# Kernel optimization log

Measured on AMD Instinct MI355X. Metric: run time of the kernel, lower is better.

Reference implementation:

```python
import jax, jax.numpy as jnp
import numpy as np

NUM_USERS = 100000
NUM_BOOKS = 50000
N_NODES = NUM_USERS + NUM_BOOKS
LATENT = 64
NUM_LAYERS = 3
N_EDGES = 2400000


def setup_inputs() -> dict:
    key = jax.random.key(0)
    ks = jax.random.split(key, 12)
    edge_index = jax.random.randint(ks[0], (2, N_EDGES), 0, N_NODES)
    embedding = jax.random.normal(ks[1], (N_NODES, LATENT), dtype=jnp.float32) * 0.1
    user_features = jax.random.normal(ks[2], (NUM_USERS, 16), dtype=jnp.float32)
    book_numerical_features = jax.random.normal(ks[3], (NUM_BOOKS, 8), dtype=jnp.float32)
    book_genre_features = jax.random.normal(ks[4], (NUM_BOOKS, 32), dtype=jnp.float32)
    W_user = jax.random.normal(ks[5], (16, LATENT), dtype=jnp.float32) * 0.1
    b_user = jnp.zeros((LATENT,), dtype=jnp.float32)
    W_num = jax.random.normal(ks[6], (8, LATENT), dtype=jnp.float32) * 0.1
    b_num = jnp.zeros((LATENT,), dtype=jnp.float32)
    W_genre = jax.random.normal(ks[7], (32, LATENT), dtype=jnp.float32) * 0.1
    b_genre = jnp.zeros((LATENT,), dtype=jnp.float32)
    return {
        "edge_index": edge_index,
        "embedding": embedding,
        "user_features": user_features,
        "book_numerical_features": book_numerical_features,
        "book_genre_features": book_genre_features,
        "W_user": W_user, "b_user": b_user,
        "W_num": W_num, "b_num": b_num,
        "W_genre": W_genre, "b_genre": b_genre,
    }


def reference(edge_index, embedding, user_features, book_numerical_features,
              book_genre_features, W_user, b_user, W_num, b_num, W_genre, b_genre):
    N = embedding.shape[0]
    # feature projections fused into initial embedding (emb0)
    user_proj = user_features @ W_user + b_user                       # [Nu, D]
    book_proj = (book_numerical_features @ W_num + b_num
                 + book_genre_features @ W_genre + b_genre)           # [Nb, D]
    emb0 = embedding + jnp.concatenate([user_proj, book_proj], axis=0)  # [N, D]

    frm, to = edge_index[0], edge_index[1]
    # symmetric degree normalization: deg counts incoming edges at target nodes
    deg = jax.ops.segment_sum(jnp.ones_like(to, dtype=emb0.dtype), to, num_segments=N)
    deg_inv_sqrt = jnp.where(deg > 0, deg ** -0.5, 0.0)
    norm = deg_inv_sqrt[frm] * deg_inv_sqrt[to]                       # [E]

    # LightGCN: gather -> scale -> scatter-add, then mean over all layer outputs
    emb = emb0
    acc = emb0
    for _ in range(NUM_LAYERS):
        msg = norm[:, None] * emb[frm]                                # [E, D]
        emb = jax.ops.segment_sum(msg, to, num_segments=N)            # [N, D]
        acc = acc + emb
    out = acc / (NUM_LAYERS + 1)
    return emb0, out
```

## Files before the change

### kernel.cpp

```cpp
#include <hip/hip_runtime.h>
#include <hip/hip_bf16.h>

typedef __hip_bfloat16 bf16;

#define D 64
#define BSH 8
#define CAP 5120
#define EPB 4096
#define NPW 8


__global__ __launch_bounds__(256) void k_initcur(int* __restrict__ gcur, int nbk) {
    int i = blockIdx.x * 256 + threadIdx.x;
    if (i < nbk) gcur[i] = i * CAP;
}


__global__ __launch_bounds__(256) void k_part(const int* __restrict__ frm,
                                              const int* __restrict__ to,
                                              int* __restrict__ gcur,
                                              int* __restrict__ be, int E, int nbk) {
    __shared__ int h[1024];
    int tid = threadIdx.x;
    for (int i = tid; i < 1024; i += 256) h[i] = 0;
    __syncthreads();

    int base = blockIdx.x * EPB;
    int  f[16], bk[16], tl[16];
    bool va[16];
    #pragma unroll
    for (int k = 0; k < 16; k++) {
        int i = base + k * 256 + tid;
        va[k] = (i < E);
        int ic = va[k] ? i : 0;
        int t = to[ic];
        f[k]  = frm[ic];
        bk[k] = t >> BSH;
        tl[k] = t & 255;
        if (va[k]) atomicAdd(&h[bk[k]], 1);
    }
    __syncthreads();
    for (int b = tid; b < nbk; b += 256) {
        int c = h[b];
        h[b] = (c > 0) ? atomicAdd(&gcur[b], c) : 0;
    }
    __syncthreads();
    #pragma unroll
    for (int k = 0; k < 16; k++) {
        if (va[k]) {
            int pos = atomicAdd(&h[bk[k]], 1);
            be[pos] = (f[k] << 8) | tl[k];
        }
    }
}


__global__ void k_bscan(const int* __restrict__ gcur, int* __restrict__ bstart,
                        int* __restrict__ row_start, int nbk, int N, int E) {
    __shared__ int s[1024];
    int t = threadIdx.x;
    int x = (t < nbk) ? (gcur[t] - t * CAP) : 0;
    s[t] = x;
    __syncthreads();
    #pragma unroll
    for (int off = 1; off < 1024; off <<= 1) {
        int v = s[t] + ((t >= off) ? s[t - off] : 0);
        __syncthreads();
        s[t] = v;
        __syncthreads();
    }
    if (t < nbk) bstart[t] = s[t] - x;
    if (t == 0) row_start[N] = E;
}


__global__ __launch_bounds__(256) void k_scatter(const int* __restrict__ gcur,
                                                 const int* __restrict__ bstart,
                                                 const int* __restrict__ be,
                                                 int* __restrict__ row_start,
                                                 float* __restrict__ dis,
                                                 int* __restrict__ csr, int N) {
    __shared__ int hist[256];
    __shared__ int scn[256];
    int b = blockIdx.x;
    int t = threadIdx.x;
    hist[t] = 0;
    __syncthreads();

    int base = b * CAP;
    int cnt  = gcur[b] - base;
    for (int i = t; i < cnt; i += 256)
        atomicAdd(&hist[be[base + i] & 255], 1);
    __syncthreads();

    int d = hist[t];
    scn[t] = d;
    __syncthreads();
    #pragma unroll
    for (int off = 1; off < 256; off <<= 1) {
        int v = scn[t] + ((t >= off) ? scn[t - off] : 0);
        __syncthreads();
        scn[t] = v;
        __syncthreads();
    }
    int rs = bstart[b] + (scn[t] - d);

    int node = (b << BSH) + t;
    if (node < N) {
        row_start[node] = rs;
        dis[node] = (d > 0) ? rsqrtf((float)d) : 0.0f;
    }
    hist[t] = rs;
    __syncthreads();

    for (int i = t; i < cnt; i += 256) {
        int rec = be[base + i];
        int pos = atomicAdd(&hist[rec & 255], 1);
        csr[pos] = rec >> 8;
    }
}


__global__ __launch_bounds__(256) void k_emb0(const float* __restrict__ emb,
                       const float* __restrict__ uf,
                       const float* __restrict__ bn,
                       const float* __restrict__ bg,
                       const float* __restrict__ Wu,
                       const float* __restrict__ bu,
                       const float* __restrict__ Wn,
                       const float* __restrict__ bnb,
                       const float* __restrict__ Wg,
                       const float* __restrict__ bgb,
                       const float* __restrict__ dis,
                       float* __restrict__ out0, bf16* __restrict__ y0,
                       int N, int NU, int ublocks) {
    int lane = threadIdx.x & 63;
    int wsub = __builtin_amdgcn_readfirstlane(threadIdx.x >> 6);

    if (blockIdx.x < ublocks) {
        float w[16];
        #pragma unroll
        for (int k = 0; k < 16; k++) w[k] = Wu[k * D + lane];
        float bias = bu[lane];

        int node0 = (blockIdx.x * 4 + wsub) * NPW;
        for (int n = 0; n < NPW; n++) {
            int node = node0 + n;
            if (node >= NU) break;
            const float4* f = (const float4*)(uf + (size_t)node * 16);
            float4 f0 = f[0], f1 = f[1], f2 = f[2], f3 = f[3];
            float p = bias
                + f0.x * w[0]  + f0.y * w[1]  + f0.z * w[2]  + f0.w * w[3]
                + f1.x * w[4]  + f1.y * w[5]  + f1.z * w[6]  + f1.w * w[7]
                + f2.x * w[8]  + f2.y * w[9]  + f2.z * w[10] + f2.w * w[11]
                + f3.x * w[12] + f3.y * w[13] + f3.z * w[14] + f3.w * w[15];
            size_t idx = (size_t)node * D + lane;
            float v = emb[idx] + p;
            out0[idx] = v;
            y0[idx]   = __float2bfloat16(dis[node] * v);
        }
    } else {
        float wn[8], wg[32];
        #pragma unroll
        for (int k = 0; k < 8; k++)  wn[k] = Wn[k * D + lane];
        #pragma unroll
        for (int k = 0; k < 32; k++) wg[k] = Wg[k * D + lane];
        float bias = bnb[lane] + bgb[lane];

        int b0 = ((blockIdx.x - ublocks) * 4 + wsub) * NPW;
        for (int n = 0; n < NPW; n++) {
            int b = b0 + n;
            int node = NU + b;
            if (node >= N) break;
            const float4* fn = (const float4*)(bn + (size_t)b * 8);
            float4 n0 = fn[0], n1 = fn[1];
            const float4* fg = (const float4*)(bg + (size_t)b * 32);
            float p = bias
                + n0.x * wn[0] + n0.y * wn[1] + n0.z * wn[2] + n0.w * wn[3]
                + n1.x * wn[4] + n1.y * wn[5] + n1.z * wn[6] + n1.w * wn[7];
            #pragma unroll
            for (int q = 0; q < 8; q++) {
                float4 g = fg[q];
                p += g.x * wg[4*q]   + g.y * wg[4*q+1]
                   + g.z * wg[4*q+2] + g.w * wg[4*q+3];
            }
            size_t idx = (size_t)node * D + lane;
            float v = emb[idx] + p;
            out0[idx] = v;
            y0[idx]   = __float2bfloat16(dis[node] * v);
        }
    }
}


static __device__ __forceinline__ unsigned int pack_bf16x2(float e, float o) {
    bf16 a = __float2bfloat16(e);
    bf16 b = __float2bfloat16(o);
    unsigned short ua = __builtin_bit_cast(unsigned short, a);
    unsigned short ub = __builtin_bit_cast(unsigned short, b);
    return (unsigned int)ua | ((unsigned int)ub << 16);
}


__global__ __launch_bounds__(256) void k_prop(const int* __restrict__ row_start,
                       const int* __restrict__ csr,
                       const float* __restrict__ dis,
                       const bf16* __restrict__ y_in,
                       bf16* __restrict__ x_out,
                       bf16* __restrict__ y_out, int N) {
    int lane = threadIdx.x & 63;
    int half = lane >> 5;
    int lh   = lane & 31;
    int node = blockIdx.x * 4 + (threadIdx.x >> 6);
    if (node >= N) return;

    int s = row_start[node];
    int e = row_start[node + 1];

    const unsigned int* y32 = (const unsigned int*)y_in;
    float a0 = 0.f, a1 = 0.f;

    int i = s;
    for (; i + 16 <= e; i += 16) {
        int jv = csr[i + (lane & 15)];
        #pragma unroll
        for (int u = 0; u < 8; u++) {
            int j = __shfl(jv, 2 * u + half);
            unsigned int d = y32[((unsigned int)j << 5) + lh];
            a0 += __uint_as_float(d << 16);
            a1 += __uint_as_float(d & 0xffff0000u);
        }
    }
    if (i < e) {
        int jv = csr[min(i + (lane & 15), e - 1)];
        int rem = e - i;
        for (int u = 0; 2 * u < rem; u++) {
            int idx = 2 * u + half;
            int j = __shfl(jv, idx);
            unsigned int d = y32[((unsigned int)j << 5) + lh];
            d = (idx < rem) ? d : 0u;
            a0 += __uint_as_float(d << 16);
            a1 += __uint_as_float(d & 0xffff0000u);
        }
    }

    a0 += __shfl_xor(a0, 32);
    a1 += __shfl_xor(a1, 32);

    float dt = dis[node];
    float x0 = dt * a0;
    float x1v = dt * a1;
    unsigned int w = (unsigned int)node * 32 + lh;
    if (half == 0) {
        ((unsigned int*)x_out)[w] = pack_bf16x2(x0, x1v);
    } else {
        ((unsigned int*)y_out)[w] = pack_bf16x2(dt * x0, dt * x1v);
    }
}


__global__ __launch_bounds__(256) void k_prop_last(const int* __restrict__ row_start,
                       const int* __restrict__ csr,
                       const float* __restrict__ dis,
                       const bf16* __restrict__ y_in,
                       const float* __restrict__ out0,
                       const bf16* __restrict__ x1,
                       const bf16* __restrict__ x2,
                       float* __restrict__ out1, int N) {
    int lane = threadIdx.x & 63;
    int half = lane >> 5;
    int lh   = lane & 31;
    int node = blockIdx.x * 4 + (threadIdx.x >> 6);
    if (node >= N) return;

    int s = row_start[node];
    int e = row_start[node + 1];

    const unsigned int* y32 = (const unsigned int*)y_in;
    float a0 = 0.f, a1 = 0.f;

    int i = s;
    for (; i + 16 <= e; i += 16) {
        int jv = csr[i + (lane & 15)];
        #pragma unroll
        for (int u = 0; u < 8; u++) {
            int j = __shfl(jv, 2 * u + half);
            unsigned int d = y32[((unsigned int)j << 5) + lh];
            a0 += __uint_as_float(d << 16);
            a1 += __uint_as_float(d & 0xffff0000u);
        }
    }
    if (i < e) {
        int jv = csr[min(i + (lane & 15), e - 1)];
        int rem = e - i;
        for (int u = 0; 2 * u < rem; u++) {
            int idx = 2 * u + half;
            int j = __shfl(jv, idx);
            unsigned int d = y32[((unsigned int)j << 5) + lh];
            d = (idx < rem) ? d : 0u;
            a0 += __uint_as_float(d << 16);
            a1 += __uint_as_float(d & 0xffff0000u);
        }
    }

    a0 += __shfl_xor(a0, 32);
    a1 += __shfl_xor(a1, 32);

    float dt = dis[node];
    float x3e = dt * a0;
    float x3o = dt * a1;

    if (half == 0) {
        unsigned int w = (unsigned int)node * 32 + lh;
        float2 o0 = ((const float2*)out0)[w];
        unsigned int p1 = ((const unsigned int*)x1)[w];
        unsigned int p2 = ((const unsigned int*)x2)[w];
        float e1 = __uint_as_float(p1 << 16);
        float o1 = __uint_as_float(p1 & 0xffff0000u);
        float e2 = __uint_as_float(p2 << 16);
        float o2 = __uint_as_float(p2 & 0xffff0000u);
        float2 r;
        r.x = (o0.x + e1 + e2 + x3e) * 0.25f;
        r.y = (o0.y + o1 + o2 + x3o) * 0.25f;
        ((float2*)out1)[w] = r;
    }
}


extern "C" void kernel_launch(void* const* d_in, const int* in_sizes, int n_in,
                              void* d_out, int out_size, void* d_ws, size_t ws_size,
                              hipStream_t stream) {
    const int E  = in_sizes[0] / 2;
    const int N  = in_sizes[1] / D;
    const int NU = in_sizes[2] / 16;
    const int nbk = (N + 255) >> BSH;

    const int*   frm = (const int*)d_in[0];
    const int*   to  = frm + E;
    const float* emb = (const float*)d_in[1];
    const float* uf  = (const float*)d_in[2];
    const float* bn  = (const float*)d_in[3];
    const float* bg  = (const float*)d_in[4];
    const float* Wu  = (const float*)d_in[5];
    const float* bu  = (const float*)d_in[6];
    const float* Wn  = (const float*)d_in[7];
    const float* bnb = (const float*)d_in[8];
    const float* Wg  = (const float*)d_in[9];
    const float* bgb = (const float*)d_in[10];

    char* p = (char*)d_ws;
    const size_t ND = (size_t)N * D;
    bf16*  y0        = (bf16*)p;   p += ND * sizeof(bf16);
    bf16*  y1        = (bf16*)p;   p += ND * sizeof(bf16);
    bf16*  x1        = (bf16*)p;   p += ND * sizeof(bf16);
    bf16*  x2        = (bf16*)p;   p += ND * sizeof(bf16);
    float* dis       = (float*)p;  p += (size_t)N * sizeof(float);
    int*   row_start = (int*)p;    p += ((size_t)N + 16) * sizeof(int);
    int*   bstart    = (int*)p;    p += 1024 * sizeof(int);
    int*   gcur      = (int*)p;    p += (size_t)nbk * sizeof(int);
    int*   csr       = (int*)p;    p += (size_t)E * sizeof(int);
    int*   be        = (int*)p;    p += (size_t)nbk * CAP * sizeof(int);

    const int TB = 256;
    const int gridNode = (N + 3) / 4;
    const int gridPart = (E + EPB - 1) / EPB;

    k_initcur<<<(nbk + TB - 1) / TB, TB, 0, stream>>>(gcur, nbk);
    k_part   <<<gridPart, TB, 0, stream>>>(frm, to, gcur, be, E, nbk);
    k_bscan  <<<1, 1024, 0, stream>>>(gcur, bstart, row_start, nbk, N, E);
    k_scatter<<<nbk, TB, 0, stream>>>(gcur, bstart, be, row_start, dis, csr, N);

    float* out0 = (float*)d_out;
    float* out1 = out0 + ND;

    const int NB = N - NU;
    const int uwaves  = (NU + NPW - 1) / NPW;
    const int ublocks = (uwaves + 3) / 4;
    const int bwaves  = (NB + NPW - 1) / NPW;
    const int bblocks = (bwaves + 3) / 4;
    k_emb0<<<ublocks + bblocks, TB, 0, stream>>>(emb, uf, bn, bg, Wu, bu, Wn, bnb,
                                                 Wg, bgb, dis, out0, y0, N, NU, ublocks);

    k_prop     <<<gridNode, TB, 0, stream>>>(row_start, csr, dis, y0, x1, y1, N);
    k_prop     <<<gridNode, TB, 0, stream>>>(row_start, csr, dis, y1, x2, y0, N);
    k_prop_last<<<gridNode, TB, 0, stream>>>(row_start, csr, dis, y0, out0, x1, x2, out1, N);
}
```

Baseline: 430.0 us.

## Process four nodes per wave in propagation kernels to raise memory-level parallelism

Each wave in the propagation kernels now handles four destination nodes at once and interleaves their neighbor gathers in one lockstep loop with per-node masking. The aim is to keep more independent gather loads in flight per wave and to spread the per-node setup cost over several nodes. In exchange, every node in the group runs as many 16-edge chunks as the group's longest row, so the masked loads waste bandwidth when degrees differ. The grid shrinks four-fold and register pressure rises.

```diff
diff --git a/kernel.cpp b/kernel.cpp
--- a/kernel.cpp
+++ b/kernel.cpp
@@ -202,6 +202,57 @@
 }
 
 
+static __device__ __forceinline__ void gather4(
+        const int* __restrict__ row_start, const int* __restrict__ csr,
+        const unsigned int* __restrict__ y32, int n0, int N, int lane,
+        float (&a0)[4], float (&a1)[4]) {
+    int half = lane >> 5;
+    int lh   = lane & 31;
+    int l16  = lane & 15;
+
+    int sv[4], ev[4];
+    #pragma unroll
+    for (int g = 0; g < 4; g++) {
+        int node = min(n0 + g, N - 1);
+        sv[g] = row_start[node];
+        ev[g] = row_start[node + 1];
+        a0[g] = 0.f;
+        a1[g] = 0.f;
+    }
+
+    for (int c = 0; ; c++) {
+        int jv[4], base[4];
+        #pragma unroll
+        for (int g = 0; g < 4; g++) {
+            base[g] = sv[g] + 16 * c;
+            jv[g] = csr[min(base[g] + l16, max(ev[g] - 1, 0))];
+        }
+        #pragma unroll
+        for (int u = 0; u < 8; u++) {
+            #pragma unroll
+            for (int g = 0; g < 4; g++) {
+                int idx = 2 * u + half;
+                int j = __shfl(jv[g], idx);
+                unsigned int d = y32[((unsigned int)j << 5) + lh];
+                d = (base[g] + idx < ev[g]) ? d : 0u;
+                a0[g] += __uint_as_float(d << 16);
+                a1[g] += __uint_as_float(d & 0xffff0000u);
+            }
+        }
+        bool cont = false;
+        #pragma unroll
+        for (int g = 0; g < 4; g++) cont = cont || (base[g] + 16 < ev[g]);
+        if (!cont) break;
+    }
+
+    #pragma unroll
+    for (int g = 0; g < 4; g++) {
+        a0[g] += __shfl_xor(a0[g], 32);
+        a1[g] += __shfl_xor(a1[g], 32);
+    }
+}
+
+
 __global__ __launch_bounds__(256) void k_prop(const int* __restrict__ row_start,
                        const int* __restrict__ csr,
                        const float* __restrict__ dis,
@@ -209,52 +260,27 @@
                        bf16* __restrict__ x_out,
                        bf16* __restrict__ y_out, int N) {
     int lane = threadIdx.x & 63;
+    int n0 = (blockIdx.x * 4 + (threadIdx.x >> 6)) * 4;
+    if (n0 >= N) return;
+
+    float a0[4], a1[4];
+    gather4(row_start, csr, (const unsigned int*)y_in, n0, N, lane, a0, a1);
+
     int half = lane >> 5;
     int lh   = lane & 31;
-    int node = blockIdx.x * 4 + (threadIdx.x >> 6);
-    if (node >= N) return;
-
-    int s = row_start[node];
-    int e = row_start[node + 1];
-
-    const unsigned int* y32 = (const unsigned int*)y_in;
-    float a0 = 0.f, a1 = 0.f;
-
-    int i = s;
-    for (; i + 16 <= e; i += 16) {
-        int jv = csr[i + (lane & 15)];
-        #pragma unroll
-        for (int u = 0; u < 8; u++) {
-            int j = __shfl(jv, 2 * u + half);
-            unsigned int d = y32[((unsigned int)j << 5) + lh];
-            a0 += __uint_as_float(d << 16);
-            a1 += __uint_as_float(d & 0xffff0000u);
-        }
-    }
-    if (i < e) {
-        int jv = csr[min(i + (lane & 15), e - 1)];
-        int rem = e - i;
-        for (int u = 0; 2 * u < rem; u++) {
-            int idx = 2 * u + half;
-            int j = __shfl(jv, idx);
-            unsigned int d = y32[((unsigned int)j << 5) + lh];
-            d = (idx < rem) ? d : 0u;
-            a0 += __uint_as_float(d << 16);
-            a1 += __uint_as_float(d & 0xffff0000u);
-        }
-    }
-
-    a0 += __shfl_xor(a0, 32);
-    a1 += __shfl_xor(a1, 32);
-
-    float dt = dis[node];
-    float x0 = dt * a0;
-    float x1v = dt * a1;
-    unsigned int w = (unsigned int)node * 32 + lh;
-    if (half == 0) {
-        ((unsigned int*)x_out)[w] = pack_bf16x2(x0, x1v);
-    } else {
-        ((unsigned int*)y_out)[w] = pack_bf16x2(dt * x0, dt * x1v);
+    #pragma unroll
+    for (int g = 0; g < 4; g++) {
+        int node = n0 + g;
+        if (node >= N) break;
+        float dt = dis[node];
+        float x0  = dt * a0[g];
+        float x1v = dt * a1[g];
+        unsigned int w = (unsigned int)node * 32 + lh;
+        if (half == 0) {
+            ((unsigned int*)x_out)[w] = pack_bf16x2(x0, x1v);
+        } else {
+            ((unsigned int*)y_out)[w] = pack_bf16x2(dt * x0, dt * x1v);
+        }
     }
 }
 
@@ -268,61 +294,35 @@
                        const bf16* __restrict__ x2,
                        float* __restrict__ out1, int N) {
     int lane = threadIdx.x & 63;
+    int n0 = (blockIdx.x * 4 + (threadIdx.x >> 6)) * 4;
+    if (n0 >= N) return;
+
+    float a0[4], a1[4];
+    gather4(row_start, csr, (const unsigned int*)y_in, n0, N, lane, a0, a1);
+
     int half = lane >> 5;
     int lh   = lane & 31;
-    int node = blockIdx.x * 4 + (threadIdx.x >> 6);
-    if (node >= N) return;
-
-    int s = row_start[node];
-    int e = row_start[node + 1];
-
-    const unsigned int* y32 = (const unsigned int*)y_in;
-    float a0 = 0.f, a1 = 0.f;
-
-    int i = s;
-    for (; i + 16 <= e; i += 16) {
-        int jv = csr[i + (lane & 15)];
-        #pragma unroll
-        for (int u = 0; u < 8; u++) {
-            int j = __shfl(jv, 2 * u + half);
-            unsigned int d = y32[((unsigned int)j << 5) + lh];
-            a0 += __uint_as_float(d << 16);
-            a1 += __uint_as_float(d & 0xffff0000u);
-        }
-    }
-    if (i < e) {
-        int jv = csr[min(i + (lane & 15), e - 1)];
-        int rem = e - i;
-        for (int u = 0; 2 * u < rem; u++) {
-            int idx = 2 * u + half;
-            int j = __shfl(jv, idx);
-            unsigned int d = y32[((unsigned int)j << 5) + lh];
-            d = (idx < rem) ? d : 0u;
-            a0 += __uint_as_float(d << 16);
-            a1 += __uint_as_float(d & 0xffff0000u);
-        }
-    }
-
-    a0 += __shfl_xor(a0, 32);
-    a1 += __shfl_xor(a1, 32);
-
-    float dt = dis[node];
-    float x3e = dt * a0;
-    float x3o = dt * a1;
-
-    if (half == 0) {
-        unsigned int w = (unsigned int)node * 32 + lh;
-        float2 o0 = ((const float2*)out0)[w];
-        unsigned int p1 = ((const unsigned int*)x1)[w];
-        unsigned int p2 = ((const unsigned int*)x2)[w];
-        float e1 = __uint_as_float(p1 << 16);
-        float o1 = __uint_as_float(p1 & 0xffff0000u);
-        float e2 = __uint_as_float(p2 << 16);
-        float o2 = __uint_as_float(p2 & 0xffff0000u);
-        float2 r;
-        r.x = (o0.x + e1 + e2 + x3e) * 0.25f;
-        r.y = (o0.y + o1 + o2 + x3o) * 0.25f;
-        ((float2*)out1)[w] = r;
+    #pragma unroll
+    for (int g = 0; g < 4; g++) {
+        int node = n0 + g;
+        if (node >= N) break;
+        float dt = dis[node];
+        float x3e = dt * a0[g];
+        float x3o = dt * a1[g];
+        if (half == 0) {
+            unsigned int w = (unsigned int)node * 32 + lh;
+            float2 o0 = ((const float2*)out0)[w];
+            unsigned int p1 = ((const unsigned int*)x1)[w];
+            unsigned int p2 = ((const unsigned int*)x2)[w];
+            float e1 = __uint_as_float(p1 << 16);
+            float o1 = __uint_as_float(p1 & 0xffff0000u);
+            float e2 = __uint_as_float(p2 << 16);
+            float o2 = __uint_as_float(p2 & 0xffff0000u);
+            float2 r;
+            r.x = (o0.x + e1 + e2 + x3e) * 0.25f;
+            r.y = (o0.y + o1 + o2 + x3o) * 0.25f;
+            ((float2*)out1)[w] = r;
+        }
     }
 }
 
@@ -362,7 +362,7 @@
     int*   be        = (int*)p;    p += (size_t)nbk * CAP * sizeof(int);
 
     const int TB = 256;
-    const int gridNode = (N + 3) / 4;
+    const int gridProp = (N + 15) / 16;
     const int gridPart = (E + EPB - 1) / EPB;
 
     k_initcur<<<(nbk + TB - 1) / TB, TB, 0, stream>>>(gcur, nbk);
@@ -381,7 +381,7 @@
     k_emb0<<<ublocks + bblocks, TB, 0, stream>>>(emb, uf, bn, bg, Wu, bu, Wn, bnb,
                                                  Wg, bgb, dis, out0, y0, N, NU, ublocks);
 
-    k_prop     <<<gridNode, TB, 0, stream>>>(row_start, csr, dis, y0, x1, y1, N);
-    k_prop     <<<gridNode, TB, 0, stream>>>(row_start, csr, dis, y1, x2, y0, N);
-    k_prop_last<<<gridNode, TB, 0, stream>>>(row_start, csr, dis, y0, out0, x1, x2, out1, N);
-}
+    k_prop     <<<gridProp, TB, 0, stream>>>(row_start, csr, dis, y0, x1, y1, N);
+    k_prop     <<<gridProp, TB, 0, stream>>>(row_start, csr, dis, y1, x2, y0, N);
+    k_prop_last<<<gridProp, TB, 0, stream>>>(row_start, csr, dis, y0, out0, x1, x2, out1, N);
+}
```

Measured after the change: 389.1 us. 1.11x faster.
